# Optimization experiments

Measured on AMD Instinct MI355X. Metric: run time of the kernel, lower is better.

The kernel has to match this reference:

```python
import jax, jax.numpy as jnp
import numpy as np

NUM_HEADS = 16
HEAD_DIM = 64  # dim_qkv // num_heads


def setup_inputs() -> dict:
    key = jax.random.key(0)
    ks = jax.random.split(key, 6)
    B, N, D = 2, 2048, 1024
    s = 1.0 / np.sqrt(D)
    x = jax.random.normal(ks[0], (B, N, D), dtype=jnp.float32)
    Wq = jax.random.normal(ks[1], (D, D), dtype=jnp.float32) * s
    Wk = jax.random.normal(ks[2], (D, D), dtype=jnp.float32) * s
    Wv = jax.random.normal(ks[3], (D, D), dtype=jnp.float32) * s
    Wo = jax.random.normal(ks[4], (D, D), dtype=jnp.float32) * s
    z = jnp.zeros((D,), dtype=jnp.float32)
    return {"x": x, "Wq": Wq, "bq": z, "Wk": Wk, "bk": z,
            "Wv": Wv, "bv": z, "Wo": Wo, "bo": z}


def _split_heads(t):
    # [B, N, H*dh] -> [B, H, N, dh]
    B, N, _ = t.shape
    return t.reshape(B, N, NUM_HEADS, HEAD_DIM).transpose(0, 2, 1, 3)


def reference(x, Wq, bq, Wk, bk, Wv, bv, Wo, bo):
    q = _split_heads(x @ Wq + bq)
    k = _split_heads(x @ Wk + bk)
    v = _split_heads(x @ Wv + bv)
    scores = jnp.einsum('bhnd,bhmd->bhnm', q, k) / jnp.sqrt(
        jnp.asarray(HEAD_DIM, dtype=x.dtype))
    attn = jax.nn.softmax(scores, axis=-1)
    heads = jnp.einsum('bhnm,bhmd->bhnd', attn, v)  # [B, H, N, dh]
    B, H, N, dh = heads.shape
    merged = heads.transpose(0, 2, 1, 3).reshape(B, N, H * dh)
    # dropout is identity in deterministic/eval mode
    return merged @ Wo + bo
```

## Files before the change

### kernel.cpp

```cpp
#include <hip/hip_runtime.h>
#include <hip/hip_bf16.h>

typedef __bf16 bf16;
typedef __attribute__((ext_vector_type(8))) __bf16 bf16x8;
typedef __attribute__((ext_vector_type(4))) __bf16 bf16x4;
typedef __attribute__((ext_vector_type(4))) float f32x4;
typedef __attribute__((ext_vector_type(16))) float f32x16;
typedef unsigned int uint;

#define MFMA16(a, b, c) __builtin_amdgcn_mfma_f32_16x16x32_bf16(a, b, c, 0, 0, 0)
#define MFMA32(a, b, c) __builtin_amdgcn_mfma_f32_32x32x16_bf16(a, b, c, 0, 0, 0)

#define GLOAD_LDS(gp, lp) \
  __builtin_amdgcn_global_load_lds( \
      (const __attribute__((address_space(1))) void*)(gp), \
      (__attribute__((address_space(3))) void*)(lp), 16, 0, 0)

#define QSCALE 0.18033688011112042f

__device__ __forceinline__ uint pack2(float a, float b) {
  unsigned short x = __builtin_bit_cast(unsigned short, (bf16)a);
  unsigned short y = __builtin_bit_cast(unsigned short, (bf16)b);
  return (uint)x | ((uint)y << 16);
}

__global__ __launch_bounds__(256) void prep_kernel(
    const float* __restrict__ x, bf16* __restrict__ y,
    const float* __restrict__ W0, const float* __restrict__ W1,
    const float* __restrict__ W2, const float* __restrict__ W3,
    bf16* __restrict__ T0, bf16* __restrict__ T1,
    bf16* __restrict__ T2, bf16* __restrict__ T3) {
  const int bid = blockIdx.x;
  if (bid < 2048) {
    int i = (bid * 256 + threadIdx.x) * 8;
    float4 a = *(const float4*)(x + i);
    float4 b = *(const float4*)(x + i + 4);
    bf16x8 v;
    v[0] = (bf16)a.x; v[1] = (bf16)a.y; v[2] = (bf16)a.z; v[3] = (bf16)a.w;
    v[4] = (bf16)b.x; v[5] = (bf16)b.y; v[6] = (bf16)b.z; v[7] = (bf16)b.w;
    *(bf16x8*)(y + i) = v;
    return;
  }
  const int wq = bid - 2048;
  const int z = wq >> 10, rem = wq & 1023;
  const float* W; bf16* T;
  switch (z) {
    case 0: W = W0; T = T0; break;
    case 1: W = W1; T = T1; break;
    case 2: W = W2; T = T2; break;
    default: W = W3; T = T3; break;
  }
  const float scl = (z == 0) ? QSCALE : 1.0f;
  __shared__ float tile[32][33];
  int tx = threadIdx.x & 31;
  int ty = threadIdx.x >> 5;
  int bx = (rem & 31) * 32, by = (rem >> 5) * 32;
#pragma unroll
  for (int i = 0; i < 32; i += 8)
    tile[ty + i][tx] = W[(size_t)(by + ty + i) * 1024 + bx + tx];
  __syncthreads();
#pragma unroll
  for (int i = 0; i < 32; i += 8)
    T[(size_t)(bx + ty + i) * 1024 + by + tx] = (bf16)(tile[tx][ty + i] * scl);
}

__global__ __launch_bounds__(256, 2) void gemm_qkv_kernel(
    const bf16* __restrict__ A, const bf16* __restrict__ Bt,
    const float* __restrict__ b0, const float* __restrict__ b1,
    const float* __restrict__ b2, bf16* __restrict__ o0,
    bf16* __restrict__ o1, bf16* __restrict__ o2) {
  __shared__ bf16 As[128 * 64];
  __shared__ bf16 Bs[128 * 64];
  const int f = blockIdx.y * 24 + blockIdx.x;
  const int wg = (f % 8) * 96 + f / 8;
  const int bn = wg % 24, bm = wg / 24;
  const int t = threadIdx.x;
  const int lane = t & 63, wid = t >> 6;
  const int wy = wid >> 1, wx = wid & 1;
  const int lr = lane & 15, lg = lane >> 4;
  const bf16* Arow = A + (size_t)bm * 128 * 1024;
  const bf16* Brow = Bt + (size_t)bn * 128 * 1024;
  f32x4 acc[4][4] = {};

  for (int k0 = 0; k0 < 1024; k0 += 64) {
    __syncthreads();
#pragma unroll
    for (int i = 0; i < 4; i++) {
      int off = i * 256 + t;
      int row = off >> 3, ch = off & 7;
      int gch = ch ^ (row & 7);
      GLOAD_LDS(Arow + (size_t)row * 1024 + k0 + gch * 8, As + off * 8);
    }
#pragma unroll
    for (int i = 0; i < 4; i++) {
      int off = i * 256 + t;
      int row = off >> 3, ch = off & 7;
      int gch = ch ^ (row & 7);
      GLOAD_LDS(Brow + (size_t)row * 1024 + k0 + gch * 8, Bs + off * 8);
    }
    __syncthreads();
#pragma unroll
    for (int kh = 0; kh < 2; kh++) {
      bf16x8 af[4], bfr[4];
#pragma unroll
      for (int i = 0; i < 4; i++) {
        int row = wy * 64 + i * 16 + lr;
        int c = kh * 4 + lg;
        af[i] = *(const bf16x8*)(As + row * 64 + ((c ^ (row & 7)) << 3));
      }
#pragma unroll
      for (int j = 0; j < 4; j++) {
        int row = wx * 64 + j * 16 + lr;
        int c = kh * 4 + lg;
        bfr[j] = *(const bf16x8*)(Bs + row * 64 + ((c ^ (row & 7)) << 3));
      }
#pragma unroll
      for (int i = 0; i < 4; i++)
#pragma unroll
        for (int j = 0; j < 4; j++)
          acc[i][j] = MFMA16(af[i], bfr[j], acc[i][j]);
    }
  }

  const int seg = bn >> 3;
  const float* bias = (seg == 0) ? b0 : (seg == 1 ? b1 : b2);
  const float bscale = (seg == 0) ? QSCALE : 1.0f;

#pragma unroll
  for (int i = 0; i < 4; i++) {
    const int rowb = bm * 128 + wy * 64 + i * 16 + lg * 4;
#pragma unroll
    for (int j = 0; j < 4; j++) {
      const int np = bn * 128 + wx * 64 + j * 16 + lr;
      const int col = np & 1023;
      const float bv = bias[col] * bscale;
      const int h = col >> 6, d = col & 63;
      const int bb = rowb >> 11, nn = rowb & 2047;
      if (seg == 2) {
        bf16x4 pk;
#pragma unroll
        for (int r = 0; r < 4; r++) pk[r] = (bf16)(acc[i][j][r] + bv);
        *(bf16x4*)(o2 + (((size_t)bb * 16 + h) * 64 + d) * 2048 + nn) = pk;
      } else {
        bf16* dst = (seg == 0) ? o0 : o1;
#pragma unroll
        for (int r = 0; r < 4; r++)
          dst[(((size_t)bb * 16 + h) * 2048 + nn + r) * 64 + d] =
              (bf16)(acc[i][j][r] + bv);
      }
    }
  }
}

__global__ __launch_bounds__(256, 2) void gemmo_kernel(
    const bf16* __restrict__ A, const bf16* __restrict__ Bt,
    const float* __restrict__ bias, float* __restrict__ out) {
  __shared__ bf16 As[128 * 64];
  __shared__ bf16 Bs[64 * 64];
  const int f = blockIdx.y * 16 + blockIdx.x;
  const int wg = (f & 7) * 64 + (f >> 3);
  const int bn = wg & 15, bm = wg >> 4;
  const int t = threadIdx.x;
  const int lane = t & 63, wid = t >> 6;
  const int wy = wid >> 1, wx = wid & 1;
  const int lr = lane & 15, lg = lane >> 4;
  const bf16* Arow = A + (size_t)bm * 128 * 1024;
  const bf16* Brow = Bt + (size_t)bn * 64 * 1024;
  f32x4 acc[4][2] = {};

  for (int k0 = 0; k0 < 1024; k0 += 64) {
    __syncthreads();
#pragma unroll
    for (int i = 0; i < 4; i++) {
      int off = i * 256 + t;
      int row = off >> 3, ch = off & 7;
      int gch = ch ^ (row & 7);
      GLOAD_LDS(Arow + (size_t)row * 1024 + k0 + gch * 8, As + off * 8);
    }
#pragma unroll
    for (int i = 0; i < 2; i++) {
      int off = i * 256 + t;
      int row = off >> 3, ch = off & 7;
      int gch = ch ^ (row & 7);
      GLOAD_LDS(Brow + (size_t)row * 1024 + k0 + gch * 8, Bs + off * 8);
    }
    __syncthreads();
#pragma unroll
    for (int kh = 0; kh < 2; kh++) {
      bf16x8 af[4], bfr[2];
#pragma unroll
      for (int i = 0; i < 4; i++) {
        int row = wy * 64 + i * 16 + lr;
        int c = kh * 4 + lg;
        af[i] = *(const bf16x8*)(As + row * 64 + ((c ^ (row & 7)) << 3));
      }
#pragma unroll
      for (int j = 0; j < 2; j++) {
        int row = wx * 32 + j * 16 + lr;
        int c = kh * 4 + lg;
        bfr[j] = *(const bf16x8*)(Bs + row * 64 + ((c ^ (row & 7)) << 3));
      }
#pragma unroll
      for (int i = 0; i < 4; i++)
#pragma unroll
        for (int j = 0; j < 2; j++)
          acc[i][j] = MFMA16(af[i], bfr[j], acc[i][j]);
    }
  }

#pragma unroll
  for (int i = 0; i < 4; i++) {
    const int rowb = bm * 128 + wy * 64 + i * 16 + lg * 4;
#pragma unroll
    for (int j = 0; j < 2; j++) {
      const int col = bn * 64 + wx * 32 + j * 16 + lr;
      const float bv = bias[col];
#pragma unroll
      for (int r = 0; r < 4; r++)
        out[(size_t)(rowb + r) * 1024 + col] = acc[i][j][r] + bv;
    }
  }
}

__global__ __launch_bounds__(512, 4) void attn_kernel(
    const bf16* __restrict__ Q, const bf16* __restrict__ K,
    const bf16* __restrict__ Vt, bf16* __restrict__ Mg) {
  __shared__ bf16 Kl[2][2][4096];
  __shared__ bf16 Vl[2][2][4096];
  const int t = threadIdx.x;
  const int lane = t & 63, w = t >> 6;
  const int half = w >> 2, wq = w & 3;
  const int l31 = lane & 31, hi = lane >> 5;
  const int f = blockIdx.y * 16 + blockIdx.x;
  const int xcd = f & 7, slot = f >> 3;
  const int bh = xcd * 4 + (slot >> 4);
  const int bx = slot & 15;
  const int b = bh >> 4, h = bh & 15;
  const bf16* Qh = Q + (size_t)bh * 2048 * 64;
  const bf16* KhH = K + (size_t)bh * 2048 * 64 + (size_t)half * 1024 * 64;
  const bf16* VhH = Vt + (size_t)bh * 64 * 2048 + half * 1024;
  const int q_row = bx * 128 + wq * 32 + l31;

  bf16x8 qf[4];
#pragma unroll
  for (int dblk = 0; dblk < 4; dblk++)
    qf[dblk] = *(const bf16x8*)(Qh + (size_t)q_row * 64 + dblk * 16 + hi * 8);

  bf16x8 onesA;
  {
    bf16 ov = (l31 == 0) ? (bf16)1.0f : (bf16)0.0f;
#pragma unroll
    for (int e = 0; e < 8; e++) onesA[e] = ov;
  }

  f32x16 o0 = {}, o1 = {}, osum = {};
  const int th = t & 255;

#define STAGE_KV(kt_, buf_)                                                   \
  {                                                                           \
    _Pragma("unroll") for (int i = 0; i < 2; i++) {                           \
      int off = i * 256 + th;                                                 \
      int row = off >> 3, ch = off & 7;                                       \
      int gch = ch ^ (row & 7);                                               \
      GLOAD_LDS(KhH + (size_t)(kt_) * 4096 + row * 64 + gch * 8,              \
                &Kl[half][buf_][off * 8]);                                    \
      GLOAD_LDS(VhH + (size_t)row * 2048 + (kt_) * 64 + gch * 8,              \
                &Vl[half][buf_][off * 8]);                                    \
    }                                                                         \
  }

  STAGE_KV(0, 0);
  __syncthreads();

  for (int kt = 0; kt < 16; kt++) {
    const int cur = kt & 1;
    if (kt < 15) STAGE_KV(kt + 1, cur ^ 1);

    f32x16 s0 = {}, s1 = {};
    __builtin_amdgcn_s_setprio(1);
#pragma unroll
    for (int dblk = 0; dblk < 4; dblk++) {
      const int c = dblk * 2 + hi;
      const int r0 = l31, r1 = 32 + l31;
      bf16x8 kf0 = *(const bf16x8*)&Kl[half][cur][r0 * 64 + ((c ^ (r0 & 7)) << 3)];
      bf16x8 kf1 = *(const bf16x8*)&Kl[half][cur][r1 * 64 + ((c ^ (r1 & 7)) << 3)];
      s0 = MFMA32(kf0, qf[dblk], s0);
      s1 = MFMA32(kf1, qf[dblk], s1);
    }
    __builtin_amdgcn_s_setprio(0);

#pragma unroll
    for (int r = 0; r < 16; r++) {
      s0[r] = __builtin_amdgcn_exp2f(s0[r]);
      s1[r] = __builtin_amdgcn_exp2f(s1[r]);
    }

    uint prc[8], prd[8];
#pragma unroll
    for (int si = 0; si < 4; si++) {
      prc[si] = pack2(s0[4 * si + 0], s0[4 * si + 1]);
      prd[si] = pack2(s0[4 * si + 2], s0[4 * si + 3]);
      prc[4 + si] = pack2(s1[4 * si + 0], s1[4 * si + 1]);
      prd[4 + si] = pack2(s1[4 * si + 2], s1[4 * si + 3]);
    }

    __builtin_amdgcn_s_setprio(1);
#pragma unroll
    for (int kbl = 0; kbl < 4; kbl++) {
      const int sb = (kbl >> 1) * 4 + (kbl & 1) * 2;
      auto rc = __builtin_amdgcn_permlane32_swap(prc[sb], prc[sb + 1], false, false);
      auto rd = __builtin_amdgcn_permlane32_swap(prd[sb], prd[sb + 1], false, false);
      union { uint u[4]; bf16x8 v; } pf;
      pf.u[0] = rc[0];
      pf.u[1] = rd[0];
      pf.u[2] = rc[1];
      pf.u[3] = rd[1];

      const int c = kbl * 2 + hi;
      const int r0 = l31, r1 = 32 + l31;
      bf16x8 vt0 = *(const bf16x8*)&Vl[half][cur][r0 * 64 + ((c ^ (r0 & 7)) << 3)];
      bf16x8 vt1 = *(const bf16x8*)&Vl[half][cur][r1 * 64 + ((c ^ (r1 & 7)) << 3)];
      o0 = MFMA32(vt0, pf.v, o0);
      o1 = MFMA32(vt1, pf.v, o1);
      osum = MFMA32(onesA, pf.v, osum);
    }
    __builtin_amdgcn_s_setprio(0);

    __syncthreads();
  }

  uint lu = __builtin_bit_cast(uint, osum[0]);
  auto lb = __builtin_amdgcn_permlane32_swap(lu, lu, false, false);
  const float den = __builtin_bit_cast(float, (uint)lb[0]);

  float* ma = (float*)&Kl[0][0][0];
  float* mb = (float*)&Vl[0][0][0];
  const int mi = (wq * 64 + lane) * 17;
  if (half == 1) {
#pragma unroll
    for (int si = 0; si < 16; si++) {
      ma[mi + si] = o0[si];
      mb[mi + si] = o1[si];
    }
    ma[mi + 16] = den;
  }
  __syncthreads();
  if (half == 0) {
    const float inv = 1.f / (den + ma[mi + 16]);
    bf16* orow = Mg + ((size_t)b * 2048 + q_row) * 1024 + h * 64;
#pragma unroll
    for (int si = 0; si < 4; si++) {
      bf16x4 p0, p1;
#pragma unroll
      for (int r = 0; r < 4; r++) {
        p0[r] = (bf16)((o0[4 * si + r] + ma[mi + 4 * si + r]) * inv);
        p1[r] = (bf16)((o1[4 * si + r] + mb[mi + 4 * si + r]) * inv);
      }
      *(bf16x4*)(orow + si * 8 + hi * 4) = p0;
      *(bf16x4*)(orow + 32 + si * 8 + hi * 4) = p1;
    }
  }
}

extern "C" void kernel_launch(void* const* d_in, const int* in_sizes, int n_in,
                              void* d_out, int out_size, void* d_ws, size_t ws_size,
                              hipStream_t stream) {
  const float* x  = (const float*)d_in[0];
  const float* Wq = (const float*)d_in[1];
  const float* bq = (const float*)d_in[2];
  const float* Wk = (const float*)d_in[3];
  const float* bk = (const float*)d_in[4];
  const float* Wv = (const float*)d_in[5];
  const float* bv = (const float*)d_in[6];
  const float* Wo = (const float*)d_in[7];
  const float* bo = (const float*)d_in[8];
  float* out = (float*)d_out;
  char* ws = (char*)d_ws;
  const size_t MiB = 1u << 20;

  bf16* Xb   = (bf16*)(ws);
  bf16* Mg   = Xb;
  bf16* Wqkv = (bf16*)(ws + 8 * MiB);
  bf16* WoT  = (bf16*)(ws + 14 * MiB);
  bf16* Qb   = (bf16*)(ws + 16 * MiB);
  bf16* Kb   = (bf16*)(ws + 24 * MiB);
  bf16* Vtb  = (bf16*)(ws + 32 * MiB);

  prep_kernel<<<6144, 256, 0, stream>>>(
      x, Xb, Wq, Wk, Wv, Wo, Wqkv, Wqkv + (1u << 20), Wqkv + (2u << 20), WoT);
  gemm_qkv_kernel<<<dim3(24, 32), 256, 0, stream>>>(
      Xb, Wqkv, bq, bk, bv, Qb, Kb, Vtb);
  attn_kernel<<<dim3(16, 32), 512, 0, stream>>>(Qb, Kb, Vtb, Mg);
  gemmo_kernel<<<dim3(16, 32), 256, 0, stream>>>(Mg, WoT, bo, out);
  (void)in_sizes; (void)n_in; (void)out_size; (void)ws_size;
}
```

Baseline: 110.0 us.

## Give each attention wave two query tiles and compute row sums on VALU

Attention blocks shrink from 512 to 256 threads. Each wave now handles two 32-row query tiles (64 rows), so every K/V fragment read from LDS feeds twice as many MFMAs. The extra MFMA that computed softmax denominators against a ones vector is replaced by per-lane VALU sums of the exponentials plus a cross-half shuffle. The cost is higher register pressure from four score and four output accumulators, fewer waves per block to hide latency, and each thread issuing twice as many staging loads.

```diff
diff --git a/kernel.cpp b/kernel.cpp
--- a/kernel.cpp
+++ b/kernel.cpp
@@ -222,14 +222,14 @@
   }
 }
 
-__global__ __launch_bounds__(512, 4) void attn_kernel(
+__global__ __launch_bounds__(256, 2) void attn_kernel(
     const bf16* __restrict__ Q, const bf16* __restrict__ K,
     const bf16* __restrict__ Vt, bf16* __restrict__ Mg) {
   __shared__ bf16 Kl[2][2][4096];
   __shared__ bf16 Vl[2][2][4096];
   const int t = threadIdx.x;
   const int lane = t & 63, w = t >> 6;
-  const int half = w >> 2, wq = w & 3;
+  const int half = w >> 1, wq = w & 1;
   const int l31 = lane & 31, hi = lane >> 5;
   const int f = blockIdx.y * 16 + blockIdx.x;
   const int xcd = f & 7, slot = f >> 3;
@@ -239,27 +239,24 @@
   const bf16* Qh = Q + (size_t)bh * 2048 * 64;
   const bf16* KhH = K + (size_t)bh * 2048 * 64 + (size_t)half * 1024 * 64;
   const bf16* VhH = Vt + (size_t)bh * 64 * 2048 + half * 1024;
-  const int q_row = bx * 128 + wq * 32 + l31;
-
-  bf16x8 qf[4];
-#pragma unroll
-  for (int dblk = 0; dblk < 4; dblk++)
-    qf[dblk] = *(const bf16x8*)(Qh + (size_t)q_row * 64 + dblk * 16 + hi * 8);
-
-  bf16x8 onesA;
-  {
-    bf16 ov = (l31 == 0) ? (bf16)1.0f : (bf16)0.0f;
-#pragma unroll
-    for (int e = 0; e < 8; e++) onesA[e] = ov;
-  }
-
-  f32x16 o0 = {}, o1 = {}, osum = {};
-  const int th = t & 255;
+  const int qA = bx * 128 + wq * 64 + l31;
+  const int qB = qA + 32;
+
+  bf16x8 qfA[4], qfB[4];
+#pragma unroll
+  for (int dblk = 0; dblk < 4; dblk++) {
+    qfA[dblk] = *(const bf16x8*)(Qh + (size_t)qA * 64 + dblk * 16 + hi * 8);
+    qfB[dblk] = *(const bf16x8*)(Qh + (size_t)qB * 64 + dblk * 16 + hi * 8);
+  }
+
+  f32x16 oA0 = {}, oA1 = {}, oB0 = {}, oB1 = {};
+  float lA = 0.f, lB = 0.f;
+  const int th = t & 127;
 
 #define STAGE_KV(kt_, buf_)                                                   \
   {                                                                           \
-    _Pragma("unroll") for (int i = 0; i < 2; i++) {                           \
-      int off = i * 256 + th;                                                 \
+    _Pragma("unroll") for (int i = 0; i < 4; i++) {                           \
+      int off = i * 128 + th;                                                 \
       int row = off >> 3, ch = off & 7;                                       \
       int gch = ch ^ (row & 7);                                               \
       GLOAD_LDS(KhH + (size_t)(kt_) * 4096 + row * 64 + gch * 8,              \
@@ -276,7 +273,7 @@
     const int cur = kt & 1;
     if (kt < 15) STAGE_KV(kt + 1, cur ^ 1);
 
-    f32x16 s0 = {}, s1 = {};
+    f32x16 sA0 = {}, sA1 = {}, sB0 = {}, sB1 = {};
     __builtin_amdgcn_s_setprio(1);
 #pragma unroll
     for (int dblk = 0; dblk < 4; dblk++) {
@@ -284,80 +281,101 @@
       const int r0 = l31, r1 = 32 + l31;
       bf16x8 kf0 = *(const bf16x8*)&Kl[half][cur][r0 * 64 + ((c ^ (r0 & 7)) << 3)];
       bf16x8 kf1 = *(const bf16x8*)&Kl[half][cur][r1 * 64 + ((c ^ (r1 & 7)) << 3)];
-      s0 = MFMA32(kf0, qf[dblk], s0);
-      s1 = MFMA32(kf1, qf[dblk], s1);
+      sA0 = MFMA32(kf0, qfA[dblk], sA0);
+      sA1 = MFMA32(kf1, qfA[dblk], sA1);
+      sB0 = MFMA32(kf0, qfB[dblk], sB0);
+      sB1 = MFMA32(kf1, qfB[dblk], sB1);
     }
     __builtin_amdgcn_s_setprio(0);
 
+    float rsA0 = 0.f, rsA1 = 0.f, rsB0 = 0.f, rsB1 = 0.f;
 #pragma unroll
     for (int r = 0; r < 16; r++) {
-      s0[r] = __builtin_amdgcn_exp2f(s0[r]);
-      s1[r] = __builtin_amdgcn_exp2f(s1[r]);
-    }
-
-    uint prc[8], prd[8];
+      sA0[r] = __builtin_amdgcn_exp2f(sA0[r]); rsA0 += sA0[r];
+      sA1[r] = __builtin_amdgcn_exp2f(sA1[r]); rsA1 += sA1[r];
+      sB0[r] = __builtin_amdgcn_exp2f(sB0[r]); rsB0 += sB0[r];
+      sB1[r] = __builtin_amdgcn_exp2f(sB1[r]); rsB1 += sB1[r];
+    }
+    lA += rsA0 + rsA1;
+    lB += rsB0 + rsB1;
+
+    uint prcA[8], prdA[8], prcB[8], prdB[8];
 #pragma unroll
     for (int si = 0; si < 4; si++) {
-      prc[si] = pack2(s0[4 * si + 0], s0[4 * si + 1]);
-      prd[si] = pack2(s0[4 * si + 2], s0[4 * si + 3]);
-      prc[4 + si] = pack2(s1[4 * si + 0], s1[4 * si + 1]);
-      prd[4 + si] = pack2(s1[4 * si + 2], s1[4 * si + 3]);
+      prcA[si] = pack2(sA0[4 * si + 0], sA0[4 * si + 1]);
+      prdA[si] = pack2(sA0[4 * si + 2], sA0[4 * si + 3]);
+      prcA[4 + si] = pack2(sA1[4 * si + 0], sA1[4 * si + 1]);
+      prdA[4 + si] = pack2(sA1[4 * si + 2], sA1[4 * si + 3]);
+      prcB[si] = pack2(sB0[4 * si + 0], sB0[4 * si + 1]);
+      prdB[si] = pack2(sB0[4 * si + 2], sB0[4 * si + 3]);
+      prcB[4 + si] = pack2(sB1[4 * si + 0], sB1[4 * si + 1]);
+      prdB[4 + si] = pack2(sB1[4 * si + 2], sB1[4 * si + 3]);
     }
 
     __builtin_amdgcn_s_setprio(1);
 #pragma unroll
     for (int kbl = 0; kbl < 4; kbl++) {
       const int sb = (kbl >> 1) * 4 + (kbl & 1) * 2;
-      auto rc = __builtin_amdgcn_permlane32_swap(prc[sb], prc[sb + 1], false, false);
-      auto rd = __builtin_amdgcn_permlane32_swap(prd[sb], prd[sb + 1], false, false);
-      union { uint u[4]; bf16x8 v; } pf;
-      pf.u[0] = rc[0];
-      pf.u[1] = rd[0];
-      pf.u[2] = rc[1];
-      pf.u[3] = rd[1];
+      auto rcA = __builtin_amdgcn_permlane32_swap(prcA[sb], prcA[sb + 1], false, false);
+      auto rdA = __builtin_amdgcn_permlane32_swap(prdA[sb], prdA[sb + 1], false, false);
+      auto rcB = __builtin_amdgcn_permlane32_swap(prcB[sb], prcB[sb + 1], false, false);
+      auto rdB = __builtin_amdgcn_permlane32_swap(prdB[sb], prdB[sb + 1], false, false);
+      union { uint u[4]; bf16x8 v; } pfA, pfB;
+      pfA.u[0] = rcA[0]; pfA.u[1] = rdA[0]; pfA.u[2] = rcA[1]; pfA.u[3] = rdA[1];
+      pfB.u[0] = rcB[0]; pfB.u[1] = rdB[0]; pfB.u[2] = rcB[1]; pfB.u[3] = rdB[1];
 
       const int c = kbl * 2 + hi;
       const int r0 = l31, r1 = 32 + l31;
       bf16x8 vt0 = *(const bf16x8*)&Vl[half][cur][r0 * 64 + ((c ^ (r0 & 7)) << 3)];
       bf16x8 vt1 = *(const bf16x8*)&Vl[half][cur][r1 * 64 + ((c ^ (r1 & 7)) << 3)];
-      o0 = MFMA32(vt0, pf.v, o0);
-      o1 = MFMA32(vt1, pf.v, o1);
-      osum = MFMA32(onesA, pf.v, osum);
+      oA0 = MFMA32(vt0, pfA.v, oA0);
+      oA1 = MFMA32(vt1, pfA.v, oA1);
+      oB0 = MFMA32(vt0, pfB.v, oB0);
+      oB1 = MFMA32(vt1, pfB.v, oB1);
     }
     __builtin_amdgcn_s_setprio(0);
 
     __syncthreads();
   }
 
-  uint lu = __builtin_bit_cast(uint, osum[0]);
-  auto lb = __builtin_amdgcn_permlane32_swap(lu, lu, false, false);
-  const float den = __builtin_bit_cast(float, (uint)lb[0]);
+  lA += __shfl_xor(lA, 32);
+  lB += __shfl_xor(lB, 32);
 
   float* ma = (float*)&Kl[0][0][0];
   float* mb = (float*)&Vl[0][0][0];
-  const int mi = (wq * 64 + lane) * 17;
+  const int miA = ((0 * 2 + wq) * 64 + lane) * 17;
+  const int miB = ((1 * 2 + wq) * 64 + lane) * 17;
   if (half == 1) {
 #pragma unroll
     for (int si = 0; si < 16; si++) {
-      ma[mi + si] = o0[si];
-      mb[mi + si] = o1[si];
-    }
-    ma[mi + 16] = den;
+      ma[miA + si] = oA0[si];
+      mb[miA + si] = oA1[si];
+      ma[miB + si] = oB0[si];
+      mb[miB + si] = oB1[si];
+    }
+    ma[miA + 16] = lA;
+    ma[miB + 16] = lB;
   }
   __syncthreads();
   if (half == 0) {
-    const float inv = 1.f / (den + ma[mi + 16]);
-    bf16* orow = Mg + ((size_t)b * 2048 + q_row) * 1024 + h * 64;
+    const float invA = 1.f / (lA + ma[miA + 16]);
+    const float invB = 1.f / (lB + ma[miB + 16]);
+    bf16* orowA = Mg + ((size_t)b * 2048 + qA) * 1024 + h * 64;
+    bf16* orowB = Mg + ((size_t)b * 2048 + qB) * 1024 + h * 64;
 #pragma unroll
     for (int si = 0; si < 4; si++) {
-      bf16x4 p0, p1;
+      bf16x4 pA0, pA1, pB0, pB1;
 #pragma unroll
       for (int r = 0; r < 4; r++) {
-        p0[r] = (bf16)((o0[4 * si + r] + ma[mi + 4 * si + r]) * inv);
-        p1[r] = (bf16)((o1[4 * si + r] + mb[mi + 4 * si + r]) * inv);
-      }
-      *(bf16x4*)(orow + si * 8 + hi * 4) = p0;
-      *(bf16x4*)(orow + 32 + si * 8 + hi * 4) = p1;
+        pA0[r] = (bf16)((oA0[4 * si + r] + ma[miA + 4 * si + r]) * invA);
+        pA1[r] = (bf16)((oA1[4 * si + r] + mb[miA + 4 * si + r]) * invA);
+        pB0[r] = (bf16)((oB0[4 * si + r] + ma[miB + 4 * si + r]) * invB);
+        pB1[r] = (bf16)((oB1[4 * si + r] + mb[miB + 4 * si + r]) * invB);
+      }
+      *(bf16x4*)(orowA + si * 8 + hi * 4) = pA0;
+      *(bf16x4*)(orowA + 32 + si * 8 + hi * 4) = pA1;
+      *(bf16x4*)(orowB + si * 8 + hi * 4) = pB0;
+      *(bf16x4*)(orowB + 32 + si * 8 + hi * 4) = pB1;
     }
   }
 }
@@ -390,7 +408,7 @@
       x, Xb, Wq, Wk, Wv, Wo, Wqkv, Wqkv + (1u << 20), Wqkv + (2u << 20), WoT);
   gemm_qkv_kernel<<<dim3(24, 32), 256, 0, stream>>>(
       Xb, Wqkv, bq, bk, bv, Qb, Kb, Vtb);
-  attn_kernel<<<dim3(16, 32), 512, 0, stream>>>(Qb, Kb, Vtb, Mg);
+  attn_kernel<<<dim3(16, 32), 256, 0, stream>>>(Qb, Kb, Vtb, Mg);
   gemmo_kernel<<<dim3(16, 32), 256, 0, stream>>>(Mg, WoT, bo, out);
   (void)in_sizes; (void)n_in; (void)out_size; (void)ws_size;
 }
```

Result: slower. 113.3 us (+3.1%).

## Software-pipeline QK^T of next tile with softmax and PV of current tile

Applied to the files above, without the earlier changes.

Restructures the attention main loop so the QK^T MFMAs and V fragment loads for the next KV tile are issued before the exp, pack and PV work of the current tile, using two register sets in a 2x-unrolled loop. Blocks shrink from 512 to 256 threads, each covering 64 query rows, and the grid doubles. Launch bounds are relaxed to allow more registers per thread. The aim is to overlap matrix-core work with the transcendental and permute work, at the cost of higher register pressure and fewer waves per block.

```diff
diff --git a/kernel.cpp b/kernel.cpp
--- a/kernel.cpp
+++ b/kernel.cpp
@@ -222,24 +222,25 @@
   }
 }
 
-__global__ __launch_bounds__(512, 4) void attn_kernel(
+__global__ __launch_bounds__(256, 2) void attn_kernel(
     const bf16* __restrict__ Q, const bf16* __restrict__ K,
     const bf16* __restrict__ Vt, bf16* __restrict__ Mg) {
   __shared__ bf16 Kl[2][2][4096];
   __shared__ bf16 Vl[2][2][4096];
   const int t = threadIdx.x;
   const int lane = t & 63, w = t >> 6;
-  const int half = w >> 2, wq = w & 3;
+  const int half = w >> 1, wq = w & 1;
   const int l31 = lane & 31, hi = lane >> 5;
-  const int f = blockIdx.y * 16 + blockIdx.x;
+  const int f = blockIdx.y * 32 + blockIdx.x;
   const int xcd = f & 7, slot = f >> 3;
-  const int bh = xcd * 4 + (slot >> 4);
-  const int bx = slot & 15;
+  const int bh = xcd * 4 + (slot >> 5);
+  const int bx = slot & 31;
   const int b = bh >> 4, h = bh & 15;
   const bf16* Qh = Q + (size_t)bh * 2048 * 64;
   const bf16* KhH = K + (size_t)bh * 2048 * 64 + (size_t)half * 1024 * 64;
   const bf16* VhH = Vt + (size_t)bh * 64 * 2048 + half * 1024;
-  const int q_row = bx * 128 + wq * 32 + l31;
+  const int q_row = bx * 64 + wq * 32 + l31;
+  const int r0 = l31, r1 = 32 + l31;
 
   bf16x8 qf[4];
 #pragma unroll
@@ -254,12 +255,12 @@
   }
 
   f32x16 o0 = {}, o1 = {}, osum = {};
-  const int th = t & 255;
+  const int th = t & 127;
 
 #define STAGE_KV(kt_, buf_)                                                   \
   {                                                                           \
-    _Pragma("unroll") for (int i = 0; i < 2; i++) {                           \
-      int off = i * 256 + th;                                                 \
+    _Pragma("unroll") for (int i = 0; i < 4; i++) {                           \
+      int off = i * 128 + th;                                                 \
       int row = off >> 3, ch = off & 7;                                       \
       int gch = ch ^ (row & 7);                                               \
       GLOAD_LDS(KhH + (size_t)(kt_) * 4096 + row * 64 + gch * 8,              \
@@ -269,64 +270,87 @@
     }                                                                         \
   }
 
+#define PRELOAD(buf_, s0_, s1_, v0_, v1_)                                     \
+  {                                                                           \
+    s0_ = (f32x16){};                                                         \
+    s1_ = (f32x16){};                                                         \
+    __builtin_amdgcn_s_setprio(1);                                            \
+    _Pragma("unroll") for (int dblk = 0; dblk < 4; dblk++) {                  \
+      const int c = dblk * 2 + hi;                                            \
+      bf16x8 kf0 =                                                            \
+          *(const bf16x8*)&Kl[half][buf_][r0 * 64 + ((c ^ (r0 & 7)) << 3)];   \
+      bf16x8 kf1 =                                                            \
+          *(const bf16x8*)&Kl[half][buf_][r1 * 64 + ((c ^ (r1 & 7)) << 3)];   \
+      s0_ = MFMA32(kf0, qf[dblk], s0_);                                       \
+      s1_ = MFMA32(kf1, qf[dblk], s1_);                                       \
+    }                                                                         \
+    __builtin_amdgcn_s_setprio(0);                                            \
+    _Pragma("unroll") for (int kbl = 0; kbl < 4; kbl++) {                     \
+      const int c = kbl * 2 + hi;                                             \
+      v0_[kbl] =                                                              \
+          *(const bf16x8*)&Vl[half][buf_][r0 * 64 + ((c ^ (r0 & 7)) << 3)];   \
+      v1_[kbl] =                                                              \
+          *(const bf16x8*)&Vl[half][buf_][r1 * 64 + ((c ^ (r1 & 7)) << 3)];   \
+    }                                                                         \
+  }
+
+#define CONSUME(s0_, s1_, v0_, v1_)                                           \
+  {                                                                           \
+    _Pragma("unroll") for (int r = 0; r < 16; r++) {                          \
+      s0_[r] = __builtin_amdgcn_exp2f(s0_[r]);                                \
+      s1_[r] = __builtin_amdgcn_exp2f(s1_[r]);                                \
+    }                                                                         \
+    uint prc[8], prd[8];                                                      \
+    _Pragma("unroll") for (int si = 0; si < 4; si++) {                        \
+      prc[si] = pack2(s0_[4 * si + 0], s0_[4 * si + 1]);                      \
+      prd[si] = pack2(s0_[4 * si + 2], s0_[4 * si + 3]);                      \
+      prc[4 + si] = pack2(s1_[4 * si + 0], s1_[4 * si + 1]);                  \
+      prd[4 + si] = pack2(s1_[4 * si + 2], s1_[4 * si + 3]);                  \
+    }                                                                         \
+    __builtin_amdgcn_s_setprio(1);                                            \
+    _Pragma("unroll") for (int kbl = 0; kbl < 4; kbl++) {                     \
+      const int sb = (kbl >> 1) * 4 + (kbl & 1) * 2;                          \
+      auto rc =                                                               \
+          __builtin_amdgcn_permlane32_swap(prc[sb], prc[sb + 1], false, false);\
+      auto rd =                                                               \
+          __builtin_amdgcn_permlane32_swap(prd[sb], prd[sb + 1], false, false);\
+      union { uint u[4]; bf16x8 v; } pf;                                      \
+      pf.u[0] = rc[0];                                                        \
+      pf.u[1] = rd[0];                                                        \
+      pf.u[2] = rc[1];                                                        \
+      pf.u[3] = rd[1];                                                        \
+      o0 = MFMA32(v0_[kbl], pf.v, o0);                                        \
+      o1 = MFMA32(v1_[kbl], pf.v, o1);                                        \
+      osum = MFMA32(onesA, pf.v, osum);                                       \
+    }                                                                         \
+    __builtin_amdgcn_s_setprio(0);                                            \
+  }
+
+  f32x16 sa0, sa1, sb0, sb1;
+  bf16x8 va0[4], va1[4], vb0[4], vb1[4];
+
   STAGE_KV(0, 0);
   __syncthreads();
-
-  for (int kt = 0; kt < 16; kt++) {
-    const int cur = kt & 1;
-    if (kt < 15) STAGE_KV(kt + 1, cur ^ 1);
-
-    f32x16 s0 = {}, s1 = {};
-    __builtin_amdgcn_s_setprio(1);
-#pragma unroll
-    for (int dblk = 0; dblk < 4; dblk++) {
-      const int c = dblk * 2 + hi;
-      const int r0 = l31, r1 = 32 + l31;
-      bf16x8 kf0 = *(const bf16x8*)&Kl[half][cur][r0 * 64 + ((c ^ (r0 & 7)) << 3)];
-      bf16x8 kf1 = *(const bf16x8*)&Kl[half][cur][r1 * 64 + ((c ^ (r1 & 7)) << 3)];
-      s0 = MFMA32(kf0, qf[dblk], s0);
-      s1 = MFMA32(kf1, qf[dblk], s1);
-    }
-    __builtin_amdgcn_s_setprio(0);
-
-#pragma unroll
-    for (int r = 0; r < 16; r++) {
-      s0[r] = __builtin_amdgcn_exp2f(s0[r]);
-      s1[r] = __builtin_amdgcn_exp2f(s1[r]);
-    }
-
-    uint prc[8], prd[8];
-#pragma unroll
-    for (int si = 0; si < 4; si++) {
-      prc[si] = pack2(s0[4 * si + 0], s0[4 * si + 1]);
-      prd[si] = pack2(s0[4 * si + 2], s0[4 * si + 3]);
-      prc[4 + si] = pack2(s1[4 * si + 0], s1[4 * si + 1]);
-      prd[4 + si] = pack2(s1[4 * si + 2], s1[4 * si + 3]);
-    }
-
-    __builtin_amdgcn_s_setprio(1);
-#pragma unroll
-    for (int kbl = 0; kbl < 4; kbl++) {
-      const int sb = (kbl >> 1) * 4 + (kbl & 1) * 2;
-      auto rc = __builtin_amdgcn_permlane32_swap(prc[sb], prc[sb + 1], false, false);
-      auto rd = __builtin_amdgcn_permlane32_swap(prd[sb], prd[sb + 1], false, false);
-      union { uint u[4]; bf16x8 v; } pf;
-      pf.u[0] = rc[0];
-      pf.u[1] = rd[0];
-      pf.u[2] = rc[1];
-      pf.u[3] = rd[1];
-
-      const int c = kbl * 2 + hi;
-      const int r0 = l31, r1 = 32 + l31;
-      bf16x8 vt0 = *(const bf16x8*)&Vl[half][cur][r0 * 64 + ((c ^ (r0 & 7)) << 3)];
-      bf16x8 vt1 = *(const bf16x8*)&Vl[half][cur][r1 * 64 + ((c ^ (r1 & 7)) << 3)];
-      o0 = MFMA32(vt0, pf.v, o0);
-      o1 = MFMA32(vt1, pf.v, o1);
-      osum = MFMA32(onesA, pf.v, osum);
-    }
-    __builtin_amdgcn_s_setprio(0);
-
-    __syncthreads();
+  PRELOAD(0, sa0, sa1, va0, va1);
+  STAGE_KV(1, 1);
+  __syncthreads();
+
+#pragma unroll 1
+  for (int kt2 = 0; kt2 < 16; kt2 += 2) {
+    {
+      const int kt = kt2;
+      if (kt < 15) PRELOAD((kt + 1) & 1, sb0, sb1, vb0, vb1);
+      if (kt < 14) STAGE_KV(kt + 2, kt & 1);
+      CONSUME(sa0, sa1, va0, va1);
+      __syncthreads();
+    }
+    {
+      const int kt = kt2 + 1;
+      if (kt < 15) PRELOAD((kt + 1) & 1, sa0, sa1, va0, va1);
+      if (kt < 14) STAGE_KV(kt + 2, kt & 1);
+      CONSUME(sb0, sb1, vb0, vb1);
+      __syncthreads();
+    }
   }
 
   uint lu = __builtin_bit_cast(uint, osum[0]);
@@ -390,7 +414,7 @@
       x, Xb, Wq, Wk, Wv, Wo, Wqkv, Wqkv + (1u << 20), Wqkv + (2u << 20), WoT);
   gemm_qkv_kernel<<<dim3(24, 32), 256, 0, stream>>>(
       Xb, Wqkv, bq, bk, bv, Qb, Kb, Vtb);
-  attn_kernel<<<dim3(16, 32), 512, 0, stream>>>(Qb, Kb, Vtb, Mg);
+  attn_kernel<<<dim3(32, 32), 256, 0, stream>>>(Qb, Kb, Vtb, Mg);
   gemmo_kernel<<<dim3(16, 32), 256, 0, stream>>>(Mg, WoT, bo, out);
   (void)in_sizes; (void)n_in; (void)out_size; (void)ws_size;
 }
```

Result: slower. 126.7 us (+15.2%).
